# Kernel optimization log

Measured on AMD Instinct MI355X. Metric: run time of the kernel, lower is better.

## Reference

```python
import jax, jax.numpy as jnp
import numpy as np

N = 6144
F_IN, H1, H2, EMB = 512, 256, 128, 64
ALPHA = 0.2  # LeakyReLU negative slope
NEG_INF = -9e15


def setup_inputs() -> dict:
    key = jax.random.key(0)
    ks = jax.random.split(key, 12)
    x = jax.random.normal(ks[0], (N, F_IN), dtype=jnp.float32)
    adj = (jax.random.uniform(ks[1], (N, N)) < 0.01).astype(jnp.float32)
    adj = jnp.maximum(adj, jnp.eye(N, dtype=jnp.float32))
    M = jax.random.uniform(ks[2], (N, N), dtype=jnp.float32)

    def glorot(k, shape):
        lim = float(np.sqrt(6.0 / (shape[0] + shape[1])))
        return jax.random.uniform(k, shape, jnp.float32, -lim, lim)

    params = {
        "W1": glorot(ks[3], (F_IN, H1)), "a_s1": glorot(ks[4], (H1, 1)), "a_n1": glorot(ks[5], (H1, 1)),
        "W2": glorot(ks[6], (H1, H2)),  "a_s2": glorot(ks[7], (H2, 1)), "a_n2": glorot(ks[8], (H2, 1)),
        "W3": glorot(ks[9], (H2, EMB)), "a_s3": glorot(ks[10], (EMB, 1)), "a_n3": glorot(ks[11], (EMB, 1)),
    }
    return {"x": x, "adj": adj, "M": M, **params}


def _gat_layer(x, adj, M, W, a_s, a_n):
    h = x @ W                                   # [N, d_out]
    e = (h @ a_s) + (h @ a_n).T                 # [N, N] pairwise logits
    e = jax.nn.leaky_relu(e * M, ALPHA)
    e = jnp.where(adj > 0, e, NEG_INF)
    att = jax.nn.softmax(e, axis=1)             # masked row softmax
    return jax.nn.elu(att @ h)


def reference(x, adj, M, W1, a_s1, a_n1, W2, a_s2, a_n2, W3, a_s3, a_n3):
    h = _gat_layer(x, adj, M, W1, a_s1, a_n1)
    h = _gat_layer(h, adj, M, W2, a_s2, a_n2)
    h = _gat_layer(h, adj, M, W3, a_s3, a_n3)
    z = h / jnp.maximum(jnp.linalg.norm(h, axis=1, keepdims=True), 1e-12)
    A_pred = jax.nn.sigmoid(z @ z.T)
    return (A_pred, z)
```

## Files before the change

### kernel.cpp

```cpp
#include <hip/hip_runtime.h>
#include <hip/hip_bf16.h>
#include <math.h>

#define NROW 6144
#define LRELU_ALPHA 0.2f
#define MAXD 128

typedef __attribute__((ext_vector_type(8))) __bf16 bf16x8;
typedef __attribute__((ext_vector_type(16))) float f32x16;

__global__ __launch_bounds__(256) void prep_wt(const float* __restrict__ W,
                                               __bf16* __restrict__ wh,
                                               __bf16* __restrict__ wl, int K, int D) {
  int idx = blockIdx.x * 256 + threadIdx.x;
  if (idx >= K * D) return;
  int k = idx / D, d = idx - k * D;
  float v = W[idx];
  __bf16 h = (__bf16)v;
  float r = v - (float)h;
  wh[(size_t)d * K + k] = h;
  wl[(size_t)d * K + k] = (__bf16)r;
}

__global__ __launch_bounds__(256) void gemm_mfma(const float* __restrict__ A,
                                                 const __bf16* __restrict__ Bth,
                                                 const __bf16* __restrict__ Btl,
                                                 float* __restrict__ C, int K, int D) {
  const int wv = threadIdx.x >> 6, lane = threadIdx.x & 63;
  const int l31 = lane & 31, lh = lane >> 5;
  const int ib = blockIdx.x * 64 + (wv >> 1) * 32;
  const int jb = blockIdx.y * 64 + (wv & 1) * 32;
  const float* Arow = A + (size_t)(ib + l31) * K + lh * 8;
  const __bf16* Bh = Bth + (size_t)(jb + l31) * K + lh * 8;
  const __bf16* Bl = Btl + (size_t)(jb + l31) * K + lh * 8;
  f32x16 acc;
#pragma unroll
  for (int r = 0; r < 16; ++r) acc[r] = 0.f;
  for (int k = 0; k < K; k += 16) {
    float4 a0 = *(const float4*)(Arow + k);
    float4 a1 = *(const float4*)(Arow + k + 4);
    bf16x8 bh = *(const bf16x8*)(Bh + k);
    bf16x8 bl = *(const bf16x8*)(Bl + k);
    float av[8] = {a0.x, a0.y, a0.z, a0.w, a1.x, a1.y, a1.z, a1.w};
    bf16x8 ah, al;
#pragma unroll
    for (int t = 0; t < 8; ++t) {
      __bf16 h = (__bf16)av[t];
      ah[t] = h;
      al[t] = (__bf16)(av[t] - (float)h);
    }
    acc = __builtin_amdgcn_mfma_f32_32x32x16_bf16(ah, bh, acc, 0, 0, 0);
    acc = __builtin_amdgcn_mfma_f32_32x32x16_bf16(ah, bl, acc, 0, 0, 0);
    acc = __builtin_amdgcn_mfma_f32_32x32x16_bf16(al, bh, acc, 0, 0, 0);
  }
#pragma unroll
  for (int r = 0; r < 16; ++r) {
    int rowi = (r & 3) + 8 * (r >> 2) + 4 * lh;
    C[(size_t)(ib + rowi) * D + jb + l31] = acc[r];
  }
}

__global__ __launch_bounds__(256) void build_csr(const float* __restrict__ adj,
                                                 const float* __restrict__ Mm,
                                                 int* __restrict__ cnt,
                                                 int* __restrict__ cidx,
                                                 float* __restrict__ cmval) {
  const int row = blockIdx.x;
  const int wv = threadIdx.x >> 6, lane = threadIdx.x & 63;
  __shared__ int wcnt[4];
  __shared__ int js[MAXD];
  const float4* arow = (const float4*)(adj + (size_t)row * NROW);
  const float* mrow = Mm + (size_t)row * NROW;
  float4 a[6];
#pragma unroll
  for (int it = 0; it < 6; ++it) a[it] = arow[wv * 384 + it * 64 + lane];
  int pc = 0;
#pragma unroll
  for (int it = 0; it < 6; ++it)
    pc += (a[it].x > 0.f) + (a[it].y > 0.f) + (a[it].z > 0.f) + (a[it].w > 0.f);
#pragma unroll
  for (int off = 32; off; off >>= 1) pc += __shfl_xor(pc, off);
  if (lane == 0) wcnt[wv] = pc;
  __syncthreads();
  int base = 0;
  for (int w = 0; w < wv; ++w) base += wcnt[w];
  const int total = min(wcnt[0] + wcnt[1] + wcnt[2] + wcnt[3], MAXD);
  const unsigned long long lmask = (1ull << lane) - 1ull;
#pragma unroll
  for (int it = 0; it < 6; ++it) {
    const int j = wv * 1536 + it * 256 + lane * 4;
    unsigned long long m;
    m = __ballot(a[it].x > 0.f);
    if (a[it].x > 0.f) { int p = base + __popcll(m & lmask); if (p < MAXD) js[p] = j; }
    base += __popcll(m);
    m = __ballot(a[it].y > 0.f);
    if (a[it].y > 0.f) { int p = base + __popcll(m & lmask); if (p < MAXD) js[p] = j + 1; }
    base += __popcll(m);
    m = __ballot(a[it].z > 0.f);
    if (a[it].z > 0.f) { int p = base + __popcll(m & lmask); if (p < MAXD) js[p] = j + 2; }
    base += __popcll(m);
    m = __ballot(a[it].w > 0.f);
    if (a[it].w > 0.f) { int p = base + __popcll(m & lmask); if (p < MAXD) js[p] = j + 3; }
    base += __popcll(m);
  }
  __syncthreads();
  for (int k = threadIdx.x; k < total; k += 256) {
    int j = js[k];
    cidx[(size_t)row * MAXD + k] = j;
    cmval[(size_t)row * MAXD + k] = mrow[j];
  }
  if (threadIdx.x == 0) cnt[row] = total;
}

__global__ __launch_bounds__(256) void sn_kernel(const float* __restrict__ h,
                                                 const float* __restrict__ a_s,
                                                 const float* __restrict__ a_n,
                                                 float* __restrict__ sv,
                                                 float* __restrict__ nv, int D) {
  int row = blockIdx.x * 4 + (threadIdx.x >> 6);
  int lane = threadIdx.x & 63;
  const float* hr = h + (size_t)row * D;
  float accs = 0.f, accn = 0.f;
  for (int d = lane; d < D; d += 64) {
    float hv = hr[d];
    accs = fmaf(hv, a_s[d], accs);
    accn = fmaf(hv, a_n[d], accn);
  }
  for (int off = 32; off; off >>= 1) {
    accs += __shfl_down(accs, off);
    accn += __shfl_down(accn, off);
  }
  if (lane == 0) { sv[row] = accs; nv[row] = accn; }
}

template <int D>
__global__ __launch_bounds__(256) void attn_csr(const float* __restrict__ h,
                                                const int* __restrict__ cnt,
                                                const int* __restrict__ cidx,
                                                const float* __restrict__ cmval,
                                                const float* __restrict__ sv,
                                                const float* __restrict__ nv,
                                                float* __restrict__ out) {
  __shared__ float ws[4][MAXD];
  __shared__ int js[4][MAXD];
  const int wv = threadIdx.x >> 6, lane = threadIdx.x & 63;
  const int row = blockIdx.x * 4 + wv;
  const int c = cnt[row];
  const float si = sv[row];
  const size_t cb = (size_t)row * MAXD;

  float e0 = -1e30f, e1 = -1e30f;
  int j0 = 0, j1 = 0;
  if (lane < c) {
    j0 = cidx[cb + lane];
    float v = (si + nv[j0]) * cmval[cb + lane];
    e0 = v > 0.f ? v : LRELU_ALPHA * v;
  }
  if (lane + 64 < c) {
    j1 = cidx[cb + lane + 64];
    float v = (si + nv[j1]) * cmval[cb + lane + 64];
    e1 = v > 0.f ? v : LRELU_ALPHA * v;
  }
  float mx = fmaxf(e0, e1);
#pragma unroll
  for (int off = 32; off; off >>= 1) mx = fmaxf(mx, __shfl_xor(mx, off));
  float w0 = lane < c ? __expf(e0 - mx) : 0.f;
  float w1 = lane + 64 < c ? __expf(e1 - mx) : 0.f;
  float s = w0 + w1;
#pragma unroll
  for (int off = 32; off; off >>= 1) s += __shfl_xor(s, off);
  const float inv = 1.f / s;
  ws[wv][lane] = w0 * inv;
  ws[wv][lane + 64] = w1 * inv;
  js[wv][lane] = j0;
  js[wv][lane + 64] = j1;
  float acc[D / 64];
#pragma unroll
  for (int q = 0; q < D / 64; ++q) acc[q] = 0.f;
#pragma unroll 4
  for (int k = 0; k < c; ++k) {
    const float wk = ws[wv][k];
    const float* hr = h + (size_t)js[wv][k] * D;
#pragma unroll
    for (int q = 0; q < D / 64; ++q) acc[q] = fmaf(wk, hr[lane + q * 64], acc[q]);
  }
#pragma unroll
  for (int q = 0; q < D / 64; ++q) {
    float a = acc[q];
    out[(size_t)row * D + lane + q * 64] = a > 0.f ? a : expm1f(a);
  }
}

__global__ __launch_bounds__(256) void norm_kernel(const float* __restrict__ h,
                                                   float* __restrict__ z,
                                                   __bf16* __restrict__ zb) {
  int row = blockIdx.x * 4 + (threadIdx.x >> 6);
  int lane = threadIdx.x & 63;
  float v = h[(size_t)row * 64 + lane];
  float sq = v * v;
  for (int off = 32; off; off >>= 1) sq += __shfl_xor(sq, off);
  float nrm = fmaxf(sqrtf(sq), 1e-12f);
  float zv = v / nrm;
  z[(size_t)row * 64 + lane] = zv;
  zb[(size_t)row * 64 + lane] = (__bf16)zv;
}

__global__ __launch_bounds__(256) void decoder_mfma(const __bf16* __restrict__ zb,
                                                    float* __restrict__ out) {
  const int wv = threadIdx.x >> 6, lane = threadIdx.x & 63;
  const int ib = blockIdx.y * 64 + (wv >> 1) * 32;
  const int jb = blockIdx.x * 64 + (wv & 1) * 32;
  const int l31 = lane & 31, lh = lane >> 5;
  const __bf16* Arow = zb + (size_t)(ib + l31) * 64 + lh * 8;
  const __bf16* Brow = zb + (size_t)(jb + l31) * 64 + lh * 8;
  f32x16 acc;
#pragma unroll
  for (int r = 0; r < 16; ++r) acc[r] = 0.f;
#pragma unroll
  for (int kk = 0; kk < 4; ++kk) {
    bf16x8 af = *(const bf16x8*)(Arow + kk * 16);
    bf16x8 bfv = *(const bf16x8*)(Brow + kk * 16);
    acc = __builtin_amdgcn_mfma_f32_32x32x16_bf16(af, bfv, acc, 0, 0, 0);
  }
#pragma unroll
  for (int r = 0; r < 16; ++r) {
    int rowi = (r & 3) + 8 * (r >> 2) + 4 * lh;
    float v = 1.f / (1.f + __expf(-acc[r]));
    out[(size_t)(ib + rowi) * NROW + jb + l31] = v;
  }
}

extern "C" void kernel_launch(void* const* d_in, const int* in_sizes, int n_in,
                              void* d_out, int out_size, void* d_ws, size_t ws_size,
                              hipStream_t stream) {
  const float* x   = (const float*)d_in[0];
  const float* adj = (const float*)d_in[1];
  const float* Mm  = (const float*)d_in[2];
  const float* W1  = (const float*)d_in[3];
  const float* as1 = (const float*)d_in[4];
  const float* an1 = (const float*)d_in[5];
  const float* W2  = (const float*)d_in[6];
  const float* as2 = (const float*)d_in[7];
  const float* an2 = (const float*)d_in[8];
  const float* W3  = (const float*)d_in[9];
  const float* as3 = (const float*)d_in[10];
  const float* an3 = (const float*)d_in[11];

  float* out = (float*)d_out;
  float* z = out + (size_t)NROW * NROW;

  float* ws = (float*)d_ws;
  float* hA   = ws;
  float* hB   = hA + (size_t)NROW * 256;
  float* sv   = hB + (size_t)NROW * 256;
  float* nv   = sv + NROW;
  float* cmv  = nv + NROW;
  int*   cix  = (int*)(cmv + (size_t)NROW * MAXD);
  int*   cct  = cix + (size_t)NROW * MAXD;
  __bf16* zb  = (__bf16*)(cct + NROW);
  __bf16* w1h = zb + (size_t)NROW * 64;
  __bf16* w1l = w1h + 512 * 256;
  __bf16* w2h = w1l + 512 * 256;
  __bf16* w2l = w2h + 256 * 128;
  __bf16* w3h = w2l + 256 * 128;
  __bf16* w3l = w3h + 128 * 64;

  dim3 b256(256);

  build_csr<<<dim3(NROW), b256, 0, stream>>>(adj, Mm, cct, cix, cmv);
  prep_wt<<<dim3(512 * 256 / 256), b256, 0, stream>>>(W1, w1h, w1l, 512, 256);
  prep_wt<<<dim3(256 * 128 / 256), b256, 0, stream>>>(W2, w2h, w2l, 256, 128);
  prep_wt<<<dim3(128 * 64 / 256), b256, 0, stream>>>(W3, w3h, w3l, 128, 64);

  gemm_mfma<<<dim3(NROW / 64, 256 / 64), b256, 0, stream>>>(x, w1h, w1l, hA, 512, 256);
  sn_kernel<<<dim3(NROW / 4), b256, 0, stream>>>(hA, as1, an1, sv, nv, 256);
  attn_csr<256><<<dim3(NROW / 4), b256, 0, stream>>>(hA, cct, cix, cmv, sv, nv, hB);

  gemm_mfma<<<dim3(NROW / 64, 128 / 64), b256, 0, stream>>>(hB, w2h, w2l, hA, 256, 128);
  sn_kernel<<<dim3(NROW / 4), b256, 0, stream>>>(hA, as2, an2, sv, nv, 128);
  attn_csr<128><<<dim3(NROW / 4), b256, 0, stream>>>(hA, cct, cix, cmv, sv, nv, hB);

  gemm_mfma<<<dim3(NROW / 64, 64 / 64), b256, 0, stream>>>(hB, w3h, w3l, hA, 128, 64);
  sn_kernel<<<dim3(NROW / 4), b256, 0, stream>>>(hA, as3, an3, sv, nv, 64);
  attn_csr<64><<<dim3(NROW / 4), b256, 0, stream>>>(hA, cct, cix, cmv, sv, nv, hB);

  norm_kernel<<<dim3(NROW / 4), b256, 0, stream>>>(hB, z, zb);
  decoder_mfma<<<dim3(NROW / 64, NROW / 64), b256, 0, stream>>>(zb, out);
}
```

Before: 209.7 us.

## Fuse preprocessing kernels, fold attention projections into GEMM, fuse norm into attention

Merges CSR building and all weight prep into one launch. Precomputes W·a_s and W·a_n so the GEMM produces the s/n logit vectors directly from the input rows, which removes three sn_kernel passes over h. Layer 1 attention splits each row's 256 columns across two waves to raise parallelism. The L2-normalize step is fused into the last attention kernel. Launch count drops, but fp32 rounding changes because the dot products are now reassociated through the precomputed projections.

```diff
diff --git a/kernel.cpp b/kernel.cpp
--- a/kernel.cpp
+++ b/kernel.cpp
@@ -9,22 +9,108 @@
 typedef __attribute__((ext_vector_type(8))) __bf16 bf16x8;
 typedef __attribute__((ext_vector_type(16))) float f32x16;
 
-__global__ __launch_bounds__(256) void prep_wt(const float* __restrict__ W,
-                                               __bf16* __restrict__ wh,
-                                               __bf16* __restrict__ wl, int K, int D) {
-  int idx = blockIdx.x * 256 + threadIdx.x;
-  if (idx >= K * D) return;
-  int k = idx / D, d = idx - k * D;
-  float v = W[idx];
-  __bf16 h = (__bf16)v;
-  float r = v - (float)h;
-  wh[(size_t)d * K + k] = h;
-  wl[(size_t)d * K + k] = (__bf16)r;
+__global__ __launch_bounds__(256) void prep_all(
+    const float* __restrict__ adj, const float* __restrict__ Mm,
+    int* __restrict__ cnt, int* __restrict__ cidx, float* __restrict__ cmval,
+    const float* __restrict__ W1, const float* __restrict__ W2, const float* __restrict__ W3,
+    __bf16* __restrict__ w1h, __bf16* __restrict__ w1l,
+    __bf16* __restrict__ w2h, __bf16* __restrict__ w2l,
+    __bf16* __restrict__ w3h, __bf16* __restrict__ w3l,
+    const float* __restrict__ as1, const float* __restrict__ an1,
+    const float* __restrict__ as2, const float* __restrict__ an2,
+    const float* __restrict__ as3, const float* __restrict__ an3,
+    float* __restrict__ wsa1, float* __restrict__ wna1,
+    float* __restrict__ wsa2, float* __restrict__ wna2,
+    float* __restrict__ wsa3, float* __restrict__ wna3) {
+  int b = blockIdx.x;
+  if (b < NROW) {
+    const int row = b;
+    const int wv = threadIdx.x >> 6, lane = threadIdx.x & 63;
+    __shared__ int wcnt[4];
+    __shared__ int js[MAXD];
+    const float4* arow = (const float4*)(adj + (size_t)row * NROW);
+    const float* mrow = Mm + (size_t)row * NROW;
+    float4 a[6];
+#pragma unroll
+    for (int it = 0; it < 6; ++it) a[it] = arow[wv * 384 + it * 64 + lane];
+    int pc = 0;
+#pragma unroll
+    for (int it = 0; it < 6; ++it)
+      pc += (a[it].x > 0.f) + (a[it].y > 0.f) + (a[it].z > 0.f) + (a[it].w > 0.f);
+#pragma unroll
+    for (int off = 32; off; off >>= 1) pc += __shfl_xor(pc, off);
+    if (lane == 0) wcnt[wv] = pc;
+    __syncthreads();
+    int base = 0;
+    for (int w = 0; w < wv; ++w) base += wcnt[w];
+    const int total = min(wcnt[0] + wcnt[1] + wcnt[2] + wcnt[3], MAXD);
+    const unsigned long long lmask = (1ull << lane) - 1ull;
+#pragma unroll
+    for (int it = 0; it < 6; ++it) {
+      const int j = wv * 1536 + it * 256 + lane * 4;
+      unsigned long long m;
+      m = __ballot(a[it].x > 0.f);
+      if (a[it].x > 0.f) { int p = base + __popcll(m & lmask); if (p < MAXD) js[p] = j; }
+      base += __popcll(m);
+      m = __ballot(a[it].y > 0.f);
+      if (a[it].y > 0.f) { int p = base + __popcll(m & lmask); if (p < MAXD) js[p] = j + 1; }
+      base += __popcll(m);
+      m = __ballot(a[it].z > 0.f);
+      if (a[it].z > 0.f) { int p = base + __popcll(m & lmask); if (p < MAXD) js[p] = j + 2; }
+      base += __popcll(m);
+      m = __ballot(a[it].w > 0.f);
+      if (a[it].w > 0.f) { int p = base + __popcll(m & lmask); if (p < MAXD) js[p] = j + 3; }
+      base += __popcll(m);
+    }
+    __syncthreads();
+    for (int k = threadIdx.x; k < total; k += 256) {
+      int j = js[k];
+      cidx[(size_t)row * MAXD + k] = j;
+      cmval[(size_t)row * MAXD + k] = mrow[j];
+    }
+    if (threadIdx.x == 0) cnt[row] = total;
+    return;
+  }
+  b -= NROW;
+  if (b < 672) {
+    int idx = b * 256 + threadIdx.x;
+    const float* W; __bf16 *wh, *wl; int K, D;
+    if (idx < 131072) { W = W1; wh = w1h; wl = w1l; K = 512; D = 256; }
+    else if (idx < 163840) { idx -= 131072; W = W2; wh = w2h; wl = w2l; K = 256; D = 128; }
+    else { idx -= 163840; if (idx >= 8192) return; W = W3; wh = w3h; wl = w3l; K = 128; D = 64; }
+    int k = idx / D, d = idx - k * D;
+    float v = W[idx];
+    __bf16 h = (__bf16)v;
+    wh[(size_t)d * K + k] = h;
+    wl[(size_t)d * K + k] = (__bf16)(v - (float)h);
+    return;
+  }
+  b -= 672;
+  int t = b * 256 + threadIdx.x;
+  if (t < 512) {
+    float s = 0.f, n = 0.f;
+    for (int d = 0; d < 256; ++d) { float w = W1[t * 256 + d]; s = fmaf(w, as1[d], s); n = fmaf(w, an1[d], n); }
+    wsa1[t] = s; wna1[t] = n;
+  } else if (t < 768) {
+    int k = t - 512;
+    float s = 0.f, n = 0.f;
+    for (int d = 0; d < 128; ++d) { float w = W2[k * 128 + d]; s = fmaf(w, as2[d], s); n = fmaf(w, an2[d], n); }
+    wsa2[k] = s; wna2[k] = n;
+  } else if (t < 896) {
+    int k = t - 768;
+    float s = 0.f, n = 0.f;
+    for (int d = 0; d < 64; ++d) { float w = W3[k * 64 + d]; s = fmaf(w, as3[d], s); n = fmaf(w, an3[d], n); }
+    wsa3[k] = s; wna3[k] = n;
+  }
 }
 
 __global__ __launch_bounds__(256) void gemm_mfma(const float* __restrict__ A,
                                                  const __bf16* __restrict__ Bth,
                                                  const __bf16* __restrict__ Btl,
+                                                 const float* __restrict__ wsa,
+                                                 const float* __restrict__ wna,
+                                                 float* __restrict__ sv,
+                                                 float* __restrict__ nv,
                                                  float* __restrict__ C, int K, int D) {
   const int wv = threadIdx.x >> 6, lane = threadIdx.x & 63;
   const int l31 = lane & 31, lh = lane >> 5;
@@ -33,15 +119,31 @@
   const float* Arow = A + (size_t)(ib + l31) * K + lh * 8;
   const __bf16* Bh = Bth + (size_t)(jb + l31) * K + lh * 8;
   const __bf16* Bl = Btl + (size_t)(jb + l31) * K + lh * 8;
+  const bool do_sn = (blockIdx.y == 0) && ((wv & 1) == 0);
   f32x16 acc;
 #pragma unroll
   for (int r = 0; r < 16; ++r) acc[r] = 0.f;
+  float ss = 0.f, nn = 0.f;
   for (int k = 0; k < K; k += 16) {
     float4 a0 = *(const float4*)(Arow + k);
     float4 a1 = *(const float4*)(Arow + k + 4);
     bf16x8 bh = *(const bf16x8*)(Bh + k);
     bf16x8 bl = *(const bf16x8*)(Bl + k);
     float av[8] = {a0.x, a0.y, a0.z, a0.w, a1.x, a1.y, a1.z, a1.w};
+    if (do_sn) {
+      float4 s0 = *(const float4*)(wsa + k + lh * 8);
+      float4 s1 = *(const float4*)(wsa + k + lh * 8 + 4);
+      float4 n0 = *(const float4*)(wna + k + lh * 8);
+      float4 n1 = *(const float4*)(wna + k + lh * 8 + 4);
+      ss = fmaf(av[0], s0.x, ss); ss = fmaf(av[1], s0.y, ss);
+      ss = fmaf(av[2], s0.z, ss); ss = fmaf(av[3], s0.w, ss);
+      ss = fmaf(av[4], s1.x, ss); ss = fmaf(av[5], s1.y, ss);
+      ss = fmaf(av[6], s1.z, ss); ss = fmaf(av[7], s1.w, ss);
+      nn = fmaf(av[0], n0.x, nn); nn = fmaf(av[1], n0.y, nn);
+      nn = fmaf(av[2], n0.z, nn); nn = fmaf(av[3], n0.w, nn);
+      nn = fmaf(av[4], n1.x, nn); nn = fmaf(av[5], n1.y, nn);
+      nn = fmaf(av[6], n1.z, nn); nn = fmaf(av[7], n1.w, nn);
+    }
     bf16x8 ah, al;
 #pragma unroll
     for (int t = 0; t < 8; ++t) {
@@ -53,6 +155,11 @@
     acc = __builtin_amdgcn_mfma_f32_32x32x16_bf16(ah, bl, acc, 0, 0, 0);
     acc = __builtin_amdgcn_mfma_f32_32x32x16_bf16(al, bh, acc, 0, 0, 0);
   }
+  if (do_sn) {
+    ss += __shfl_xor(ss, 32);
+    nn += __shfl_xor(nn, 32);
+    if (lh == 0) { sv[ib + l31] = ss; nv[ib + l31] = nn; }
+  }
 #pragma unroll
   for (int r = 0; r < 16; ++r) {
     int rowi = (r & 3) + 8 * (r >> 2) + 4 * lh;
@@ -60,91 +167,22 @@
   }
 }
 
-__global__ __launch_bounds__(256) void build_csr(const float* __restrict__ adj,
-                                                 const float* __restrict__ Mm,
-                                                 int* __restrict__ cnt,
-                                                 int* __restrict__ cidx,
-                                                 float* __restrict__ cmval) {
-  const int row = blockIdx.x;
-  const int wv = threadIdx.x >> 6, lane = threadIdx.x & 63;
-  __shared__ int wcnt[4];
-  __shared__ int js[MAXD];
-  const float4* arow = (const float4*)(adj + (size_t)row * NROW);
-  const float* mrow = Mm + (size_t)row * NROW;
-  float4 a[6];
-#pragma unroll
-  for (int it = 0; it < 6; ++it) a[it] = arow[wv * 384 + it * 64 + lane];
-  int pc = 0;
-#pragma unroll
-  for (int it = 0; it < 6; ++it)
-    pc += (a[it].x > 0.f) + (a[it].y > 0.f) + (a[it].z > 0.f) + (a[it].w > 0.f);
-#pragma unroll
-  for (int off = 32; off; off >>= 1) pc += __shfl_xor(pc, off);
-  if (lane == 0) wcnt[wv] = pc;
-  __syncthreads();
-  int base = 0;
-  for (int w = 0; w < wv; ++w) base += wcnt[w];
-  const int total = min(wcnt[0] + wcnt[1] + wcnt[2] + wcnt[3], MAXD);
-  const unsigned long long lmask = (1ull << lane) - 1ull;
-#pragma unroll
-  for (int it = 0; it < 6; ++it) {
-    const int j = wv * 1536 + it * 256 + lane * 4;
-    unsigned long long m;
-    m = __ballot(a[it].x > 0.f);
-    if (a[it].x > 0.f) { int p = base + __popcll(m & lmask); if (p < MAXD) js[p] = j; }
-    base += __popcll(m);
-    m = __ballot(a[it].y > 0.f);
-    if (a[it].y > 0.f) { int p = base + __popcll(m & lmask); if (p < MAXD) js[p] = j + 1; }
-    base += __popcll(m);
-    m = __ballot(a[it].z > 0.f);
-    if (a[it].z > 0.f) { int p = base + __popcll(m & lmask); if (p < MAXD) js[p] = j + 2; }
-    base += __popcll(m);
-    m = __ballot(a[it].w > 0.f);
-    if (a[it].w > 0.f) { int p = base + __popcll(m & lmask); if (p < MAXD) js[p] = j + 3; }
-    base += __popcll(m);
-  }
-  __syncthreads();
-  for (int k = threadIdx.x; k < total; k += 256) {
-    int j = js[k];
-    cidx[(size_t)row * MAXD + k] = j;
-    cmval[(size_t)row * MAXD + k] = mrow[j];
-  }
-  if (threadIdx.x == 0) cnt[row] = total;
-}
-
-__global__ __launch_bounds__(256) void sn_kernel(const float* __restrict__ h,
-                                                 const float* __restrict__ a_s,
-                                                 const float* __restrict__ a_n,
-                                                 float* __restrict__ sv,
-                                                 float* __restrict__ nv, int D) {
-  int row = blockIdx.x * 4 + (threadIdx.x >> 6);
-  int lane = threadIdx.x & 63;
-  const float* hr = h + (size_t)row * D;
-  float accs = 0.f, accn = 0.f;
-  for (int d = lane; d < D; d += 64) {
-    float hv = hr[d];
-    accs = fmaf(hv, a_s[d], accs);
-    accn = fmaf(hv, a_n[d], accn);
-  }
-  for (int off = 32; off; off >>= 1) {
-    accs += __shfl_down(accs, off);
-    accn += __shfl_down(accn, off);
-  }
-  if (lane == 0) { sv[row] = accs; nv[row] = accn; }
-}
-
-template <int D>
+template <int D, int WPR, bool NORM>
 __global__ __launch_bounds__(256) void attn_csr(const float* __restrict__ h,
                                                 const int* __restrict__ cnt,
                                                 const int* __restrict__ cidx,
                                                 const float* __restrict__ cmval,
                                                 const float* __restrict__ sv,
                                                 const float* __restrict__ nv,
-                                                float* __restrict__ out) {
+                                                float* __restrict__ out,
+                                                __bf16* __restrict__ zb) {
+  constexpr int RPB = 4 / WPR;
+  constexpr int NQ = D / (64 * WPR);
   __shared__ float ws[4][MAXD];
   __shared__ int js[4][MAXD];
   const int wv = threadIdx.x >> 6, lane = threadIdx.x & 63;
-  const int row = blockIdx.x * 4 + wv;
+  const int row = blockIdx.x * RPB + wv / WPR;
+  const int half = wv % WPR;
   const int c = cnt[row];
   const float si = sv[row];
   const size_t cb = (size_t)row * MAXD;
@@ -174,35 +212,33 @@
   ws[wv][lane + 64] = w1 * inv;
   js[wv][lane] = j0;
   js[wv][lane + 64] = j1;
-  float acc[D / 64];
-#pragma unroll
-  for (int q = 0; q < D / 64; ++q) acc[q] = 0.f;
-#pragma unroll 4
+  float acc[NQ];
+#pragma unroll
+  for (int q = 0; q < NQ; ++q) acc[q] = 0.f;
+  const int cbase = half * (D / WPR);
+#pragma unroll 8
   for (int k = 0; k < c; ++k) {
     const float wk = ws[wv][k];
-    const float* hr = h + (size_t)js[wv][k] * D;
-#pragma unroll
-    for (int q = 0; q < D / 64; ++q) acc[q] = fmaf(wk, hr[lane + q * 64], acc[q]);
-  }
-#pragma unroll
-  for (int q = 0; q < D / 64; ++q) {
-    float a = acc[q];
-    out[(size_t)row * D + lane + q * 64] = a > 0.f ? a : expm1f(a);
-  }
-}
-
-__global__ __launch_bounds__(256) void norm_kernel(const float* __restrict__ h,
-                                                   float* __restrict__ z,
-                                                   __bf16* __restrict__ zb) {
-  int row = blockIdx.x * 4 + (threadIdx.x >> 6);
-  int lane = threadIdx.x & 63;
-  float v = h[(size_t)row * 64 + lane];
-  float sq = v * v;
-  for (int off = 32; off; off >>= 1) sq += __shfl_xor(sq, off);
-  float nrm = fmaxf(sqrtf(sq), 1e-12f);
-  float zv = v / nrm;
-  z[(size_t)row * 64 + lane] = zv;
-  zb[(size_t)row * 64 + lane] = (__bf16)zv;
+    const float* hr = h + (size_t)js[wv][k] * D + cbase;
+#pragma unroll
+    for (int q = 0; q < NQ; ++q) acc[q] = fmaf(wk, hr[lane + q * 64], acc[q]);
+  }
+  if (!NORM) {
+#pragma unroll
+    for (int q = 0; q < NQ; ++q) {
+      float a = acc[q];
+      out[(size_t)row * D + cbase + lane + q * 64] = a > 0.f ? a : expm1f(a);
+    }
+  } else {
+    float a = acc[0];
+    a = a > 0.f ? a : expm1f(a);
+    float sq = a * a;
+#pragma unroll
+    for (int off = 32; off; off >>= 1) sq += __shfl_xor(sq, off);
+    float zv = a / fmaxf(sqrtf(sq), 1e-12f);
+    out[(size_t)row * 64 + lane] = zv;
+    zb[(size_t)row * 64 + lane] = (__bf16)zv;
+  }
 }
 
 __global__ __launch_bounds__(256) void decoder_mfma(const __bf16* __restrict__ zb,
@@ -264,26 +300,27 @@
   __bf16* w2l = w2h + 256 * 128;
   __bf16* w3h = w2l + 256 * 128;
   __bf16* w3l = w3h + 128 * 64;
+  float* wsa1 = (float*)(w3l + 128 * 64);
+  float* wna1 = wsa1 + 512;
+  float* wsa2 = wna1 + 512;
+  float* wna2 = wsa2 + 256;
+  float* wsa3 = wna2 + 256;
+  float* wna3 = wsa3 + 128;
 
   dim3 b256(256);
 
-  build_csr<<<dim3(NROW), b256, 0, stream>>>(adj, Mm, cct, cix, cmv);
-  prep_wt<<<dim3(512 * 256 / 256), b256, 0, stream>>>(W1, w1h, w1l, 512, 256);
-  prep_wt<<<dim3(256 * 128 / 256), b256, 0, stream>>>(W2, w2h, w2l, 256, 128);
-  prep_wt<<<dim3(128 * 64 / 256), b256, 0, stream>>>(W3, w3h, w3l, 128, 64);
-
-  gemm_mfma<<<dim3(NROW / 64, 256 / 64), b256, 0, stream>>>(x, w1h, w1l, hA, 512, 256);
-  sn_kernel<<<dim3(NROW / 4), b256, 0, stream>>>(hA, as1, an1, sv, nv, 256);
-  attn_csr<256><<<dim3(NROW / 4), b256, 0, stream>>>(hA, cct, cix, cmv, sv, nv, hB);
-
-  gemm_mfma<<<dim3(NROW / 64, 128 / 64), b256, 0, stream>>>(hB, w2h, w2l, hA, 256, 128);
-  sn_kernel<<<dim3(NROW / 4), b256, 0, stream>>>(hA, as2, an2, sv, nv, 128);
-  attn_csr<128><<<dim3(NROW / 4), b256, 0, stream>>>(hA, cct, cix, cmv, sv, nv, hB);
-
-  gemm_mfma<<<dim3(NROW / 64, 64 / 64), b256, 0, stream>>>(hB, w3h, w3l, hA, 128, 64);
-  sn_kernel<<<dim3(NROW / 4), b256, 0, stream>>>(hA, as3, an3, sv, nv, 64);
-  attn_csr<64><<<dim3(NROW / 4), b256, 0, stream>>>(hA, cct, cix, cmv, sv, nv, hB);
-
-  norm_kernel<<<dim3(NROW / 4), b256, 0, stream>>>(hB, z, zb);
+  prep_all<<<dim3(NROW + 672 + 4), b256, 0, stream>>>(
+      adj, Mm, cct, cix, cmv, W1, W2, W3, w1h, w1l, w2h, w2l, w3h, w3l,
+      as1, an1, as2, an2, as3, an3, wsa1, wna1, wsa2, wna2, wsa3, wna3);
+
+  gemm_mfma<<<dim3(NROW / 64, 4), b256, 0, stream>>>(x, w1h, w1l, wsa1, wna1, sv, nv, hA, 512, 256);
+  attn_csr<256, 2, false><<<dim3(NROW / 2), b256, 0, stream>>>(hA, cct, cix, cmv, sv, nv, hB, nullptr);
+
+  gemm_mfma<<<dim3(NROW / 64, 2), b256, 0, stream>>>(hB, w2h, w2l, wsa2, wna2, sv, nv, hA, 256, 128);
+  attn_csr<128, 1, false><<<dim3(NROW / 4), b256, 0, stream>>>(hA, cct, cix, cmv, sv, nv, hB, nullptr);
+
+  gemm_mfma<<<dim3(NROW / 64, 1), b256, 0, stream>>>(hB, w3h, w3l, wsa3, wna3, sv, nv, hA, 128, 64);
+  attn_csr<64, 1, true><<<dim3(NROW / 4), b256, 0, stream>>>(hA, cct, cix, cmv, sv, nv, z, zb);
+
   decoder_mfma<<<dim3(NROW / 64, NROW / 64), b256, 0, stream>>>(zb, out);
 }
```

After: 200.2 us. -4.5%, faster.
